# Performance work log

Measured on AMD Instinct MI355X. Metric: run time of the kernel, lower is better.

## Reference

```python
import jax, jax.numpy as jnp
import numpy as np

B, T, H = 256, 512, 1024


def setup_inputs() -> dict:
    key = jax.random.key(0)
    ks = jax.random.split(key, 11)
    s = 1.0 / np.sqrt(H)
    u = lambda k, shape: jax.random.uniform(k, shape, jnp.float32, -s, s)
    return {
        "x": jax.random.normal(ks[0], (B, T), jnp.float32),
        "W_ih1": u(ks[1], (4 * H, 1)),
        "W_hh1": u(ks[2], (4 * H, H)),
        "b_ih1": u(ks[3], (4 * H,)),
        "b_hh1": u(ks[4], (4 * H,)),
        "W_ih2": u(ks[5], (4 * H, H)),
        "W_hh2": u(ks[6], (4 * H, H)),
        "b_ih2": u(ks[7], (4 * H,)),
        "b_hh2": u(ks[8], (4 * H,)),
        "W_out": u(ks[9], (1, H)),
        "b_out": u(ks[10], (1,)),
        "future": 0,
    }


def _lstm_cell(x, h, c, W_ih, W_hh, b):
    # PyTorch LSTMCell gate order: i, f, g, o
    gates = x @ W_ih.T + h @ W_hh.T + b
    i, f, g, o = jnp.split(gates, 4, axis=-1)
    c_new = jax.nn.sigmoid(f) * c + jax.nn.sigmoid(i) * jnp.tanh(g)
    h_new = jax.nn.sigmoid(o) * jnp.tanh(c_new)
    return h_new, c_new


def reference(x, W_ih1, W_hh1, b_ih1, b_hh1, W_ih2, W_hh2, b_ih2, b_hh2, W_out, b_out, future):
    Bn = x.shape[0]
    Hd = W_hh1.shape[1]
    b1 = b_ih1 + b_hh1
    b2 = b_ih2 + b_hh2

    def step(carry, x_t):
        h1, c1, h2, c2 = carry
        h1, c1 = _lstm_cell(x_t, h1, c1, W_ih1, W_hh1, b1)
        h2, c2 = _lstm_cell(h1, h2, c2, W_ih2, W_hh2, b2)
        out = h2 @ W_out.T + b_out  # [B, 1]
        return (h1, c1, h2, c2), out

    xs = x.T[:, :, None]  # [T, B, 1]
    carry0 = tuple(jnp.zeros((Bn, Hd), x.dtype) for _ in range(4))
    carry, outs = jax.lax.scan(step, carry0, xs)  # outs: [T, B, 1]
    outputs = [outs[:, :, 0].T]  # [B, T]

    # closed-loop future prediction (future is a static Python int)
    out = outs[-1]
    for _ in range(future):
        carry, out = step(carry, out)
        outputs.append(out)
    return jnp.concatenate(outputs, axis=1)
```

## Files before the change

### kernel.cpp

```cpp
#include <hip/hip_runtime.h>
#include <hip/hip_cooperative_groups.h>
#include <math.h>

namespace cg = cooperative_groups;

#define Bsz 256
#define Tsz 512
#define GSTR 130

using half8   = __attribute__((ext_vector_type(8))) _Float16;
using half2_t = __attribute__((ext_vector_type(2))) _Float16;
using f32x4   = __attribute__((ext_vector_type(4))) float;

#define MFMA(a, b, c) __builtin_amdgcn_mfma_f32_16x16x32_f16(a, b, c, 0, 0, 0)
#define INV2048 (1.0f / 2048.0f)

__device__ __forceinline__ float sigm(float v)   { return 1.0f / (1.0f + expf(-v)); }
__device__ __forceinline__ float tanh_f(float v) { float e = expf(2.0f * v); return 1.0f - 2.0f / (e + 1.0f); }

__device__ __forceinline__ void split8(const float* p, half8& hi, half8& lo) {
    float4 v0 = *(const float4*)p, v1 = *(const float4*)(p + 4);
    float vv[8] = {v0.x, v0.y, v0.z, v0.w, v1.x, v1.y, v1.z, v1.w};
    #pragma unroll
    for (int j = 0; j < 8; ++j) {
        hi[j] = (_Float16)vv[j];
        lo[j] = (_Float16)((vv[j] - (float)hi[j]) * 2048.0f);
    }
}

__device__ __forceinline__ void grid_barrier(unsigned* bar0, unsigned* bar1,
                                             int bx, unsigned target16) {
    __syncthreads();
    if (threadIdx.x == 0) {
        unsigned old = __hip_atomic_fetch_add(&bar0[(bx & 15) << 5], 1u,
                                              __ATOMIC_ACQ_REL, __HIP_MEMORY_SCOPE_AGENT);
        if ((old & 15u) == 15u)
            __hip_atomic_fetch_add(bar1, 1u, __ATOMIC_ACQ_REL, __HIP_MEMORY_SCOPE_AGENT);
        while (__hip_atomic_load(bar1, __ATOMIC_RELAXED, __HIP_MEMORY_SCOPE_AGENT) < target16)
            __builtin_amdgcn_s_sleep(2);
        (void)__hip_atomic_load(bar1, __ATOMIC_ACQUIRE, __HIP_MEMORY_SCOPE_AGENT);
    }
    __syncthreads();
}

__global__ __launch_bounds__(512, 2) void lstm_persist(
    const float* __restrict__ x,
    const float* __restrict__ W_ih1, const float* __restrict__ W_hh1,
    const float* __restrict__ b_ih1, const float* __restrict__ b_hh1,
    const float* __restrict__ W_ih2, const float* __restrict__ W_hh2,
    const float* __restrict__ b_ih2, const float* __restrict__ b_hh2,
    const float* __restrict__ W_out, const float* __restrict__ b_out,
    float* __restrict__ out, char* __restrict__ ws)
{
    __shared__ float gA[32 * GSTR];
    __shared__ float gB[32 * GSTR];
    __shared__ float poArr[4 * GSTR];
    __shared__ float b1p[32], b2p[32], wihp[32], woutp[8], bouts_s;

    cg::grid_group grid = cg::this_grid();

    const int tid  = threadIdx.x;
    const int lane = tid & 63;
    const int wv   = tid >> 6;
    const int m    = lane & 15;
    const int quad = lane >> 4;
    const int bx   = blockIdx.x;
    const int rg   = bx >> 1;
    const int BH   = bx & 1;
    const int HO   = rg << 3;

    float*    xT       = (float*)ws;
    _Float16* hswz     = (_Float16*)(ws + (512 << 10));
    float*    partials = (float*)(ws + (512 << 10) + (4 << 20));
    unsigned* bar0     = (unsigned*)(ws + (512 << 10) + (4 << 20) + (256 << 10));
    unsigned* bar1     = bar0 + 1024;

    #define HBUF(p, l, hl) (hswz + ((((p) << 2) | ((l) << 1) | (hl)) << 18))

    if (bx == 0) {
        if (tid < 16) bar0[tid << 5] = 0u;
        if (tid == 16) *bar1 = 0u;
    }
    if (tid < 32) {
        int row = ((tid & 3) << 10) + HO + (tid >> 2);
        b1p[tid]  = b_ih1[row] + b_hh1[row];
        b2p[tid]  = b_ih2[row] + b_hh2[row];
        wihp[tid] = W_ih1[row];
        if (tid < 8) woutp[tid] = W_out[HO + tid];
        if (tid == 0) bouts_s = b_out[0];
    }
    {
        const int gidx = bx * 512 + tid;
        *(float4*)((char*)hswz + (2u << 20) + (size_t)gidx * 16) = make_float4(0, 0, 0, 0);
        xT[gidx] = x[(gidx & 255) * Tsz + (gidx >> 8)];
    }

    half8 wAh[2][4], wAl[2][4], wBh[2][8], wBl[2][8];
    #pragma unroll
    for (int mt = 0; mt < 2; ++mt) {
        const int pr = (mt << 4) + m;
        const size_t rw = (size_t)(((pr & 3) << 10) + HO + (pr >> 2)) << 10;
        #pragma unroll
        for (int kt = 0; kt < 4; ++kt) {
            const int k = (wv << 7) + (kt << 5) + (quad << 3);
            split8(W_hh1 + rw + k, wAh[mt][kt], wAl[mt][kt]);
        }
        #pragma unroll
        for (int kt = 0; kt < 8; ++kt) {
            const int k = (wv << 8) + (kt << 5) + (quad << 3);
            const float* p = (k < 1024) ? (W_ih2 + rw + k) : (W_hh2 + rw + k - 1024);
            split8(p, wBh[mt][kt], wBl[mt][kt]);
        }
    }

    grid.sync();

    for (int idx = tid; idx < 4096; idx += 512) {
        const int p = idx >> 7, b = idx & 127;
        gA[p * GSTR + b] = b1p[p] + xT[(BH << 7) + b] * wihp[p];
        gB[p * GSTR + b] = b2p[p];
    }
    __syncthreads();

    float c1r[2] = {0, 0}, c2r[2] = {0, 0};
    const int b_loc = tid & 127, hp = tid >> 7;
    const int bglob = (BH << 7) + b_loc;

    for (int it = 0; it <= Tsz; ++it) {
        const int parW = it & 1;
        const int parR = parW ^ 1;

        float xnext = 0.0f;
        if (it + 1 < Tsz) xnext = xT[((it + 1) << 8) + bglob];

        if (wv == 0 && it >= 2) {
            const float* pp = partials + (parW << 15) + (bx << 7);
            float s = pp[lane] + pp[lane + 64];
            s += __shfl_xor(s, 32); s += __shfl_xor(s, 16); s += __shfl_xor(s, 8);
            s += __shfl_xor(s, 4);  s += __shfl_xor(s, 2);  s += __shfl_xor(s, 1);
            if (lane == 0) out[(bx << 9) + (it - 2)] = bouts_s + s;
        }

        if (it < Tsz) {
            const _Float16* bhB = HBUF(parR, 0, 0);
            const _Float16* blB = HBUF(parR, 0, 1);
            const int lo_off = (wv << 11) + (lane << 3);
            #pragma unroll 2
            for (int bi = 0; bi < 8; ++bi) {
                const int btl = (bi + wv) & 7;
                const _Float16* ph = bhB + (((BH << 3) + btl) << 14) + lo_off;
                const _Float16* pl = blB + (((BH << 3) + btl) << 14) + lo_off;
                f32x4 a0[2] = {(f32x4){0,0,0,0}, (f32x4){0,0,0,0}};
                f32x4 a1[2] = {(f32x4){0,0,0,0}, (f32x4){0,0,0,0}};
                #pragma unroll
                for (int kt = 0; kt < 4; ++kt) {
                    const half8 bh = *(const half8*)(ph + (kt << 9));
                    const half8 bl = *(const half8*)(pl + (kt << 9));
                    a0[0] = MFMA(wAh[0][kt], bh, a0[0]);
                    a1[0] = MFMA(wAh[0][kt], bl, a1[0]);
                    a1[0] = MFMA(wAl[0][kt], bh, a1[0]);
                    a0[1] = MFMA(wAh[1][kt], bh, a0[1]);
                    a1[1] = MFMA(wAh[1][kt], bl, a1[1]);
                    a1[1] = MFMA(wAl[1][kt], bh, a1[1]);
                }
                const int col = (btl << 4) + m;
                #pragma unroll
                for (int mt = 0; mt < 2; ++mt)
                    #pragma unroll
                    for (int r = 0; r < 4; ++r)
                        atomicAdd(&gA[((mt << 4) + (quad << 2) + r) * GSTR + col],
                                  a0[mt][r] + a1[mt][r] * INV2048);
            }
        }

        if (it >= 1) {
            const bool l2 = (wv >= 4);
            const _Float16* bhB = l2 ? HBUF(parW, 1, 0) : HBUF(parR, 0, 0);
            const _Float16* blB = l2 ? HBUF(parW, 1, 1) : HBUF(parR, 0, 1);
            const int lo_off = ((wv & 3) << 12) + (lane << 3);
            #pragma unroll 2
            for (int bi = 0; bi < 8; ++bi) {
                const int btl = (bi + wv) & 7;
                const _Float16* ph = bhB + (((BH << 3) + btl) << 14) + lo_off;
                const _Float16* pl = blB + (((BH << 3) + btl) << 14) + lo_off;
                f32x4 a0[2] = {(f32x4){0,0,0,0}, (f32x4){0,0,0,0}};
                f32x4 a1[2] = {(f32x4){0,0,0,0}, (f32x4){0,0,0,0}};
                #pragma unroll
                for (int kt = 0; kt < 8; ++kt) {
                    const half8 bh = *(const half8*)(ph + (kt << 9));
                    const half8 bl = *(const half8*)(pl + (kt << 9));
                    a0[0] = MFMA(wBh[0][kt], bh, a0[0]);
                    a1[0] = MFMA(wBh[0][kt], bl, a1[0]);
                    a1[0] = MFMA(wBl[0][kt], bh, a1[0]);
                    a0[1] = MFMA(wBh[1][kt], bh, a0[1]);
                    a1[1] = MFMA(wBh[1][kt], bl, a1[1]);
                    a1[1] = MFMA(wBl[1][kt], bh, a1[1]);
                }
                const int col = (btl << 4) + m;
                #pragma unroll
                for (int mt = 0; mt < 2; ++mt)
                    #pragma unroll
                    for (int r = 0; r < 4; ++r)
                        atomicAdd(&gB[((mt << 4) + (quad << 2) + r) * GSTR + col],
                                  a0[mt][r] + a1[mt][r] * INV2048);
            }
        }

        __syncthreads();

        if (it < Tsz) {
            half2_t hhi, hlo;
            #pragma unroll
            for (int j = 0; j < 2; ++j) {
                const int p = (hp << 3) + (j << 2);
                const float gi = gA[(p + 0) * GSTR + b_loc];
                const float gf = gA[(p + 1) * GSTR + b_loc];
                const float gg = gA[(p + 2) * GSTR + b_loc];
                const float go = gA[(p + 3) * GSTR + b_loc];
                const float c  = sigm(gf) * c1r[j] + sigm(gi) * tanh_f(gg);
                c1r[j] = c;
                const float hn = sigm(go) * tanh_f(c);
                hhi[j] = (_Float16)hn;
                hlo[j] = (_Float16)((hn - (float)hhi[j]) * 2048.0f);
            }
            const int k0 = HO + (hp << 1);
            const int wofs = ((bglob >> 4) << 14) + ((k0 >> 5) << 9)
                           + (((bglob & 15) | (((k0 >> 3) & 3) << 4)) << 3) + (k0 & 7);
            *(half2_t*)(HBUF(parW, 0, 0) + wofs) = hhi;
            *(half2_t*)(HBUF(parW, 0, 1) + wofs) = hlo;
            if (it + 1 < Tsz) {
                #pragma unroll
                for (int p = (hp << 3); p < (hp << 3) + 8; ++p)
                    gA[p * GSTR + b_loc] = b1p[p] + xnext * wihp[p];
            }
        }
        if (it >= 1) {
            half2_t hhi, hlo;
            float po = 0.0f;
            #pragma unroll
            for (int j = 0; j < 2; ++j) {
                const int p = (hp << 3) + (j << 2);
                const float gi = gB[(p + 0) * GSTR + b_loc];
                const float gf = gB[(p + 1) * GSTR + b_loc];
                const float gg = gB[(p + 2) * GSTR + b_loc];
                const float go = gB[(p + 3) * GSTR + b_loc];
                const float c  = sigm(gf) * c2r[j] + sigm(gi) * tanh_f(gg);
                c2r[j] = c;
                const float hn = sigm(go) * tanh_f(c);
                hhi[j] = (_Float16)hn;
                hlo[j] = (_Float16)((hn - (float)hhi[j]) * 2048.0f);
                po += hn * woutp[(hp << 1) + j];
            }
            const int k0 = HO + (hp << 1);
            const int wofs = ((bglob >> 4) << 14) + ((k0 >> 5) << 9)
                           + (((bglob & 15) | (((k0 >> 3) & 3) << 4)) << 3) + (k0 & 7);
            *(half2_t*)(HBUF(parR, 1, 0) + wofs) = hhi;
            *(half2_t*)(HBUF(parR, 1, 1) + wofs) = hlo;
            poArr[hp * GSTR + b_loc] = po;
            #pragma unroll
            for (int p = (hp << 3); p < (hp << 3) + 8; ++p)
                gB[p * GSTR + b_loc] = b2p[p];
        }

        __syncthreads();
        if (it >= 1 && tid < 128) {
            const float s = poArr[tid] + poArr[GSTR + tid]
                          + poArr[2 * GSTR + tid] + poArr[3 * GSTR + tid];
            partials[((it & 1) ? 0 : (1 << 15)) + (((BH << 7) + tid) << 7) + rg] = s;
        }

        grid_barrier(bar0, bar1, bx, 16u * (unsigned)(it + 1));
    }

    if (wv == 0) {
        const float* pp = partials + (1 << 15) + (bx << 7);
        float s = pp[lane] + pp[lane + 64];
        s += __shfl_xor(s, 32); s += __shfl_xor(s, 16); s += __shfl_xor(s, 8);
        s += __shfl_xor(s, 4);  s += __shfl_xor(s, 2);  s += __shfl_xor(s, 1);
        if (lane == 0) out[(bx << 9) + (Tsz - 1)] = bouts_s + s;
    }
    #undef HBUF
}

extern "C" void kernel_launch(void* const* d_in, const int* in_sizes, int n_in,
                              void* d_out, int out_size, void* d_ws, size_t ws_size,
                              hipStream_t stream)
{
    const float* x     = (const float*)d_in[0];
    const float* W_ih1 = (const float*)d_in[1];
    const float* W_hh1 = (const float*)d_in[2];
    const float* b_ih1 = (const float*)d_in[3];
    const float* b_hh1 = (const float*)d_in[4];
    const float* W_ih2 = (const float*)d_in[5];
    const float* W_hh2 = (const float*)d_in[6];
    const float* b_ih2 = (const float*)d_in[7];
    const float* b_hh2 = (const float*)d_in[8];
    const float* W_out = (const float*)d_in[9];
    const float* b_out = (const float*)d_in[10];
    float* out = (float*)d_out;
    char*  ws  = (char*)d_ws;

    void* args[] = {
        (void*)&x,
        (void*)&W_ih1, (void*)&W_hh1, (void*)&b_ih1, (void*)&b_hh1,
        (void*)&W_ih2, (void*)&W_hh2, (void*)&b_ih2, (void*)&b_hh2,
        (void*)&W_out, (void*)&b_out, (void*)&out, (void*)&ws,
    };
    hipLaunchCooperativeKernel((const void*)lstm_persist,
                               dim3(256), dim3(512), args, 0, stream);
}
```

Measured before the change: 53.59 ms.

## Split blocks by layer instead of batch half, add software-pipelined B loads

Blocks are repartitioned so the first 128 handle layer 1 and the rest handle layer 2 across the full batch of 256, instead of each block doing both layers for half the batch. This halves the weight registers per block (one layer's split-fp16 weights) and the shared-memory gate buffers, and each block now walks 16 batch tiles. The MFMA inner loop also prefetches the next k-slice of h fragments before issuing the current MFMAs. Load is imbalanced: layer-2 blocks do twice the K work of layer-1 blocks, so the slower half may set the per-step barrier time. The output partials reduction may still assume the old block-to-row mapping.

```diff
diff --git a/kernel.cpp b/kernel.cpp
--- a/kernel.cpp
+++ b/kernel.cpp
@@ -6,13 +6,13 @@
 
 #define Bsz 256
 #define Tsz 512
-#define GSTR 130
-
-using half8   = __attribute__((ext_vector_type(8))) _Float16;
-using half2_t = __attribute__((ext_vector_type(2))) _Float16;
-using f32x4   = __attribute__((ext_vector_type(4))) float;
-
-#define MFMA(a, b, c) __builtin_amdgcn_mfma_f32_16x16x32_f16(a, b, c, 0, 0, 0)
+#define GSTR 258
+
+using half8 = __attribute__((ext_vector_type(8))) _Float16;
+using half4 = __attribute__((ext_vector_type(4))) _Float16;
+using f32x4 = __attribute__((ext_vector_type(4))) float;
+
+#define MFMA_V(acc, a, b) (acc) = __builtin_amdgcn_mfma_f32_16x16x32_f16((a), (b), (acc), 0, 0, 0)
 #define INV2048 (1.0f / 2048.0f)
 
 __device__ __forceinline__ float sigm(float v)   { return 1.0f / (1.0f + expf(-v)); }
@@ -52,10 +52,10 @@
     const float* __restrict__ W_out, const float* __restrict__ b_out,
     float* __restrict__ out, char* __restrict__ ws)
 {
-    __shared__ float gA[32 * GSTR];
-    __shared__ float gB[32 * GSTR];
-    __shared__ float poArr[4 * GSTR];
-    __shared__ float b1p[32], b2p[32], wihp[32], woutp[8], bouts_s;
+    __shared__ float gAcc[32 * GSTR];
+    __shared__ float poArr[2 * GSTR];
+    __shared__ float bp[32], wihp[32], woutp[8];
+    __shared__ float bouts_s;
 
     cg::grid_group grid = cg::this_grid();
 
@@ -65,8 +65,8 @@
     const int m    = lane & 15;
     const int quad = lane >> 4;
     const int bx   = blockIdx.x;
-    const int rg   = bx >> 1;
-    const int BH   = bx & 1;
+    const bool isL2 = (bx >= 128);
+    const int rg   = isL2 ? (bx - 128) : bx;
     const int HO   = rg << 3;
 
     float*    xT       = (float*)ws;
@@ -82,11 +82,14 @@
         if (tid == 16) *bar1 = 0u;
     }
     if (tid < 32) {
-        int row = ((tid & 3) << 10) + HO + (tid >> 2);
-        b1p[tid]  = b_ih1[row] + b_hh1[row];
-        b2p[tid]  = b_ih2[row] + b_hh2[row];
-        wihp[tid] = W_ih1[row];
-        if (tid < 8) woutp[tid] = W_out[HO + tid];
+        const int row = ((tid & 3) << 10) + HO + (tid >> 2);
+        if (!isL2) {
+            bp[tid]   = b_ih1[row] + b_hh1[row];
+            wihp[tid] = W_ih1[row];
+        } else {
+            bp[tid] = b_ih2[row] + b_hh2[row];
+            if (tid < 8) woutp[tid] = W_out[HO + tid];
+        }
         if (tid == 0) bouts_s = b_out[0];
     }
     {
@@ -95,43 +98,45 @@
         xT[gidx] = x[(gidx & 255) * Tsz + (gidx >> 8)];
     }
 
-    half8 wAh[2][4], wAl[2][4], wBh[2][8], wBl[2][8];
+    half8 wh[2][8], wl[2][8];
+    const int nkt = isL2 ? 8 : 4;
     #pragma unroll
     for (int mt = 0; mt < 2; ++mt) {
         const int pr = (mt << 4) + m;
         const size_t rw = (size_t)(((pr & 3) << 10) + HO + (pr >> 2)) << 10;
-        #pragma unroll
-        for (int kt = 0; kt < 4; ++kt) {
-            const int k = (wv << 7) + (kt << 5) + (quad << 3);
-            split8(W_hh1 + rw + k, wAh[mt][kt], wAl[mt][kt]);
-        }
-        #pragma unroll
-        for (int kt = 0; kt < 8; ++kt) {
-            const int k = (wv << 8) + (kt << 5) + (quad << 3);
-            const float* p = (k < 1024) ? (W_ih2 + rw + k) : (W_hh2 + rw + k - 1024);
-            split8(p, wBh[mt][kt], wBl[mt][kt]);
+        for (int kt = 0; kt < nkt; ++kt) {
+            if (!isL2) {
+                const int k = (wv << 7) + (kt << 5) + (quad << 3);
+                split8(W_hh1 + rw + k, wh[mt][kt], wl[mt][kt]);
+            } else {
+                const int k = (wv << 8) + (kt << 5) + (quad << 3);
+                const float* p = (k < 1024) ? (W_ih2 + rw + k)
+                                            : (W_hh2 + rw + k - 1024);
+                split8(p, wh[mt][kt], wl[mt][kt]);
+            }
         }
     }
 
     grid.sync();
 
-    for (int idx = tid; idx < 4096; idx += 512) {
-        const int p = idx >> 7, b = idx & 127;
-        gA[p * GSTR + b] = b1p[p] + xT[(BH << 7) + b] * wihp[p];
-        gB[p * GSTR + b] = b2p[p];
+    for (int idx = tid; idx < 8192; idx += 512) {
+        const int p = idx >> 8, b = idx & 255;
+        gAcc[p * GSTR + b] = isL2 ? bp[p] : (bp[p] + xT[b] * wihp[p]);
     }
     __syncthreads();
 
-    float c1r[2] = {0, 0}, c2r[2] = {0, 0};
-    const int b_loc = tid & 127, hp = tid >> 7;
-    const int bglob = (BH << 7) + b_loc;
+    float cr[4] = {0, 0, 0, 0};
+    const int b_ep = tid & 255, hg = tid >> 8;
+    const int k0e  = HO + (hg << 2);
+    const int wofs = ((b_ep >> 4) << 14) + ((k0e >> 5) << 9)
+                   + (((b_ep & 15) | (((k0e >> 3) & 3) << 4)) << 3) + (k0e & 7);
 
     for (int it = 0; it <= Tsz; ++it) {
         const int parW = it & 1;
         const int parR = parW ^ 1;
 
         float xnext = 0.0f;
-        if (it + 1 < Tsz) xnext = xT[((it + 1) << 8) + bglob];
+        if (!isL2 && it + 1 < Tsz) xnext = xT[((it + 1) << 8) + b_ep];
 
         if (wv == 0 && it >= 2) {
             const float* pp = partials + (parW << 15) + (bx << 7);
@@ -141,132 +146,141 @@
             if (lane == 0) out[(bx << 9) + (it - 2)] = bouts_s + s;
         }
 
-        if (it < Tsz) {
-            const _Float16* bhB = HBUF(parR, 0, 0);
-            const _Float16* blB = HBUF(parR, 0, 1);
-            const int lo_off = (wv << 11) + (lane << 3);
-            #pragma unroll 2
-            for (int bi = 0; bi < 8; ++bi) {
-                const int btl = (bi + wv) & 7;
-                const _Float16* ph = bhB + (((BH << 3) + btl) << 14) + lo_off;
-                const _Float16* pl = blB + (((BH << 3) + btl) << 14) + lo_off;
-                f32x4 a0[2] = {(f32x4){0,0,0,0}, (f32x4){0,0,0,0}};
-                f32x4 a1[2] = {(f32x4){0,0,0,0}, (f32x4){0,0,0,0}};
+        if (!isL2) {
+            if (it < Tsz) {
+                const _Float16* bhB = HBUF(parR, 0, 0);
+                const _Float16* blB = HBUF(parR, 0, 1);
+                const int lo_off = (wv << 11) + (lane << 3);
+                #pragma unroll 2
+                for (int bi = 0; bi < 16; ++bi) {
+                    const int btl = (bi + (wv << 1)) & 15;
+                    const _Float16* ph = bhB + (btl << 14) + lo_off;
+                    const _Float16* pl = blB + (btl << 14) + lo_off;
+                    f32x4 a0[2] = {(f32x4){0,0,0,0}, (f32x4){0,0,0,0}};
+                    f32x4 a1[2] = {(f32x4){0,0,0,0}, (f32x4){0,0,0,0}};
+                    half8 bh = *(const half8*)ph;
+                    half8 bl = *(const half8*)pl;
+                    #pragma unroll
+                    for (int kt = 0; kt < 4; ++kt) {
+                        half8 bhN, blN;
+                        if (kt < 3) {
+                            bhN = *(const half8*)(ph + ((kt + 1) << 9));
+                            blN = *(const half8*)(pl + ((kt + 1) << 9));
+                        }
+                        MFMA_V(a0[0], wh[0][kt], bh);
+                        MFMA_V(a1[0], wh[0][kt], bl);
+                        MFMA_V(a1[0], wl[0][kt], bh);
+                        MFMA_V(a0[1], wh[1][kt], bh);
+                        MFMA_V(a1[1], wh[1][kt], bl);
+                        MFMA_V(a1[1], wl[1][kt], bh);
+                        bh = bhN; bl = blN;
+                    }
+                    const int col = (btl << 4) + m;
+                    #pragma unroll
+                    for (int mt = 0; mt < 2; ++mt)
+                        #pragma unroll
+                        for (int r = 0; r < 4; ++r)
+                            atomicAdd(&gAcc[((mt << 4) + (quad << 2) + r) * GSTR + col],
+                                      a0[mt][r] + a1[mt][r] * INV2048);
+                }
+            }
+        } else {
+            if (it >= 1) {
+                const bool hi2 = (wv >= 4);
+                const _Float16* bhB = hi2 ? HBUF(parW, 1, 0) : HBUF(parR, 0, 0);
+                const _Float16* blB = hi2 ? HBUF(parW, 1, 1) : HBUF(parR, 0, 1);
+                const int lo_off = ((wv & 3) << 12) + (lane << 3);
+                #pragma unroll 2
+                for (int bi = 0; bi < 16; ++bi) {
+                    const int btl = (bi + (wv << 1)) & 15;
+                    const _Float16* ph = bhB + (btl << 14) + lo_off;
+                    const _Float16* pl = blB + (btl << 14) + lo_off;
+                    f32x4 a0[2] = {(f32x4){0,0,0,0}, (f32x4){0,0,0,0}};
+                    f32x4 a1[2] = {(f32x4){0,0,0,0}, (f32x4){0,0,0,0}};
+                    half8 bh = *(const half8*)ph;
+                    half8 bl = *(const half8*)pl;
+                    #pragma unroll
+                    for (int kt = 0; kt < 8; ++kt) {
+                        half8 bhN, blN;
+                        if (kt < 7) {
+                            bhN = *(const half8*)(ph + ((kt + 1) << 9));
+                            blN = *(const half8*)(pl + ((kt + 1) << 9));
+                        }
+                        MFMA_V(a0[0], wh[0][kt], bh);
+                        MFMA_V(a1[0], wh[0][kt], bl);
+                        MFMA_V(a1[0], wl[0][kt], bh);
+                        MFMA_V(a0[1], wh[1][kt], bh);
+                        MFMA_V(a1[1], wh[1][kt], bl);
+                        MFMA_V(a1[1], wl[1][kt], bh);
+                        bh = bhN; bl = blN;
+                    }
+                    const int col = (btl << 4) + m;
+                    #pragma unroll
+                    for (int mt = 0; mt < 2; ++mt)
+                        #pragma unroll
+                        for (int r = 0; r < 4; ++r)
+                            atomicAdd(&gAcc[((mt << 4) + (quad << 2) + r) * GSTR + col],
+                                      a0[mt][r] + a1[mt][r] * INV2048);
+                }
+            }
+        }
+
+        __syncthreads();
+
+        if (!isL2) {
+            if (it < Tsz) {
+                half4 hhi, hlo;
                 #pragma unroll
-                for (int kt = 0; kt < 4; ++kt) {
-                    const half8 bh = *(const half8*)(ph + (kt << 9));
-                    const half8 bl = *(const half8*)(pl + (kt << 9));
-                    a0[0] = MFMA(wAh[0][kt], bh, a0[0]);
-                    a1[0] = MFMA(wAh[0][kt], bl, a1[0]);
-                    a1[0] = MFMA(wAl[0][kt], bh, a1[0]);
-                    a0[1] = MFMA(wAh[1][kt], bh, a0[1]);
-                    a1[1] = MFMA(wAh[1][kt], bl, a1[1]);
-                    a1[1] = MFMA(wAl[1][kt], bh, a1[1]);
-                }
-                const int col = (btl << 4) + m;
+                for (int j = 0; j < 4; ++j) {
+                    const int p = (hg << 4) + (j << 2);
+                    const float gi = gAcc[(p + 0) * GSTR + b_ep];
+                    const float gf = gAcc[(p + 1) * GSTR + b_ep];
+                    const float gg = gAcc[(p + 2) * GSTR + b_ep];
+                    const float go = gAcc[(p + 3) * GSTR + b_ep];
+                    const float c  = sigm(gf) * cr[j] + sigm(gi) * tanh_f(gg);
+                    cr[j] = c;
+                    const float hn = sigm(go) * tanh_f(c);
+                    hhi[j] = (_Float16)hn;
+                    hlo[j] = (_Float16)((hn - (float)hhi[j]) * 2048.0f);
+                }
+                *(half4*)(HBUF(parW, 0, 0) + wofs) = hhi;
+                *(half4*)(HBUF(parW, 0, 1) + wofs) = hlo;
+                if (it + 1 < Tsz) {
+                    #pragma unroll
+                    for (int p = (hg << 4); p < (hg << 4) + 16; ++p)
+                        gAcc[p * GSTR + b_ep] = bp[p] + xnext * wihp[p];
+                }
+            }
+        } else {
+            if (it >= 1) {
+                half4 hhi, hlo;
+                float po = 0.0f;
                 #pragma unroll
-                for (int mt = 0; mt < 2; ++mt)
-                    #pragma unroll
-                    for (int r = 0; r < 4; ++r)
-                        atomicAdd(&gA[((mt << 4) + (quad << 2) + r) * GSTR + col],
-                                  a0[mt][r] + a1[mt][r] * INV2048);
-            }
-        }
-
-        if (it >= 1) {
-            const bool l2 = (wv >= 4);
-            const _Float16* bhB = l2 ? HBUF(parW, 1, 0) : HBUF(parR, 0, 0);
-            const _Float16* blB = l2 ? HBUF(parW, 1, 1) : HBUF(parR, 0, 1);
-            const int lo_off = ((wv & 3) << 12) + (lane << 3);
-            #pragma unroll 2
-            for (int bi = 0; bi < 8; ++bi) {
-                const int btl = (bi + wv) & 7;
-                const _Float16* ph = bhB + (((BH << 3) + btl) << 14) + lo_off;
-                const _Float16* pl = blB + (((BH << 3) + btl) << 14) + lo_off;
-                f32x4 a0[2] = {(f32x4){0,0,0,0}, (f32x4){0,0,0,0}};
-                f32x4 a1[2] = {(f32x4){0,0,0,0}, (f32x4){0,0,0,0}};
+                for (int j = 0; j < 4; ++j) {
+                    const int p = (hg << 4) + (j << 2);
+                    const float gi = gAcc[(p + 0) * GSTR + b_ep];
+                    const float gf = gAcc[(p + 1) * GSTR + b_ep];
+                    const float gg = gAcc[(p + 2) * GSTR + b_ep];
+                    const float go = gAcc[(p + 3) * GSTR + b_ep];
+                    const float c  = sigm(gf) * cr[j] + sigm(gi) * tanh_f(gg);
+                    cr[j] = c;
+                    const float hn = sigm(go) * tanh_f(c);
+                    hhi[j] = (_Float16)hn;
+                    hlo[j] = (_Float16)((hn - (float)hhi[j]) * 2048.0f);
+                    po += hn * woutp[(hg << 2) + j];
+                }
+                *(half4*)(HBUF(parR, 1, 0) + wofs) = hhi;
+                *(half4*)(HBUF(parR, 1, 1) + wofs) = hlo;
+                poArr[hg * GSTR + b_ep] = po;
                 #pragma unroll
-                for (int kt = 0; kt < 8; ++kt) {
-                    const half8 bh = *(const half8*)(ph + (kt << 9));
-                    const half8 bl = *(const half8*)(pl + (kt << 9));
-                    a0[0] = MFMA(wBh[0][kt], bh, a0[0]);
-                    a1[0] = MFMA(wBh[0][kt], bl, a1[0]);
-                    a1[0] = MFMA(wBl[0][kt], bh, a1[0]);
-                    a0[1] = MFMA(wBh[1][kt], bh, a0[1]);
-                    a1[1] = MFMA(wBh[1][kt], bl, a1[1]);
-                    a1[1] = MFMA(wBl[1][kt], bh, a1[1]);
-                }
-                const int col = (btl << 4) + m;
-                #pragma unroll
-                for (int mt = 0; mt < 2; ++mt)
-                    #pragma unroll
-                    for (int r = 0; r < 4; ++r)
-                        atomicAdd(&gB[((mt << 4) + (quad << 2) + r) * GSTR + col],
-                                  a0[mt][r] + a1[mt][r] * INV2048);
-            }
-        }
-
-        __syncthreads();
-
-        if (it < Tsz) {
-            half2_t hhi, hlo;
-            #pragma unroll
-            for (int j = 0; j < 2; ++j) {
-                const int p = (hp << 3) + (j << 2);
-                const float gi = gA[(p + 0) * GSTR + b_loc];
-                const float gf = gA[(p + 1) * GSTR + b_loc];
-                const float gg = gA[(p + 2) * GSTR + b_loc];
-                const float go = gA[(p + 3) * GSTR + b_loc];
-                const float c  = sigm(gf) * c1r[j] + sigm(gi) * tanh_f(gg);
-                c1r[j] = c;
-                const float hn = sigm(go) * tanh_f(c);
-                hhi[j] = (_Float16)hn;
-                hlo[j] = (_Float16)((hn - (float)hhi[j]) * 2048.0f);
-            }
-            const int k0 = HO + (hp << 1);
-            const int wofs = ((bglob >> 4) << 14) + ((k0 >> 5) << 9)
-                           + (((bglob & 15) | (((k0 >> 3) & 3) << 4)) << 3) + (k0 & 7);
-            *(half2_t*)(HBUF(parW, 0, 0) + wofs) = hhi;
-            *(half2_t*)(HBUF(parW, 0, 1) + wofs) = hlo;
-            if (it + 1 < Tsz) {
-                #pragma unroll
-                for (int p = (hp << 3); p < (hp << 3) + 8; ++p)
-                    gA[p * GSTR + b_loc] = b1p[p] + xnext * wihp[p];
-            }
-        }
-        if (it >= 1) {
-            half2_t hhi, hlo;
-            float po = 0.0f;
-            #pragma unroll
-            for (int j = 0; j < 2; ++j) {
-                const int p = (hp << 3) + (j << 2);
-                const float gi = gB[(p + 0) * GSTR + b_loc];
-                const float gf = gB[(p + 1) * GSTR + b_loc];
-                const float gg = gB[(p + 2) * GSTR + b_loc];
-                const float go = gB[(p + 3) * GSTR + b_loc];
-                const float c  = sigm(gf) * c2r[j] + sigm(gi) * tanh_f(gg);
-                c2r[j] = c;
-                const float hn = sigm(go) * tanh_f(c);
-                hhi[j] = (_Float16)hn;
-                hlo[j] = (_Float16)((hn - (float)hhi[j]) * 2048.0f);
-                po += hn * woutp[(hp << 1) + j];
-            }
-            const int k0 = HO + (hp << 1);
-            const int wofs = ((bglob >> 4) << 14) + ((k0 >> 5) << 9)
-                           + (((bglob & 15) | (((k0 >> 3) & 3) << 4)) << 3) + (k0 & 7);
-            *(half2_t*)(HBUF(parR, 1, 0) + wofs) = hhi;
-            *(half2_t*)(HBUF(parR, 1, 1) + wofs) = hlo;
-            poArr[hp * GSTR + b_loc] = po;
-            #pragma unroll
-            for (int p = (hp << 3); p < (hp << 3) + 8; ++p)
-                gB[p * GSTR + b_loc] = b2p[p];
-        }
-
-        __syncthreads();
-        if (it >= 1 && tid < 128) {
-            const float s = poArr[tid] + poArr[GSTR + tid]
-                          + poArr[2 * GSTR + tid] + poArr[3 * GSTR + tid];
-            partials[((it & 1) ? 0 : (1 << 15)) + (((BH << 7) + tid) << 7) + rg] = s;
+                for (int p = (hg << 4); p < (hg << 4) + 16; ++p)
+                    gAcc[p * GSTR + b_ep] = bp[p];
+            }
+            __syncthreads();
+            if (it >= 1 && tid < 256) {
+                const float s = poArr[tid] + poArr[GSTR + tid];
+                partials[(parR << 15) + (tid << 7) + rg] = s;
+            }
         }
 
         grid_barrier(bar0, bar1, bx, 16u * (unsigned)(it + 1));
```

Result: faster. 52.32 ms (-2.4%).
